# Optimization experiments

Hardware: AMD Instinct MI355X
Metric: run time of the kernel (lower is better)

The kernel has to match this reference:

```python
import jax, jax.numpy as jnp
import numpy as np

D_MODEL = 768
N_HEADS = 12
D_KEYS = 64
D_LLM = 4096
D_INNER = N_HEADS * D_KEYS  # 768


def setup_inputs() -> dict:
    key = jax.random.key(0)
    ks = jax.random.split(key, 12)
    inp = {
        "target_embedding": jax.random.normal(ks[0], (8, 1024, D_MODEL), dtype=jnp.float32),
        "source_embedding": jax.random.normal(ks[1], (1000, D_LLM), dtype=jnp.float32),
        "value_embedding": jax.random.normal(ks[2], (1000, D_LLM), dtype=jnp.float32),
        # Linear params stored as [in, out] (y = x @ W + b)
        "Wq": jax.random.normal(ks[3], (D_MODEL, D_INNER), dtype=jnp.float32) * 0.02,
        "bq": jnp.zeros((D_INNER,), dtype=jnp.float32),
        "Wk": jax.random.normal(ks[4], (D_LLM, D_INNER), dtype=jnp.float32) * 0.02,
        "bk": jnp.zeros((D_INNER,), dtype=jnp.float32),
        "Wv": jax.random.normal(ks[5], (D_LLM, D_INNER), dtype=jnp.float32) * 0.02,
        "bv": jnp.zeros((D_INNER,), dtype=jnp.float32),
        "Wo": jax.random.normal(ks[6], (D_INNER, D_LLM), dtype=jnp.float32) * 0.02,
        "bo": jnp.zeros((D_LLM,), dtype=jnp.float32),
    }
    return inp


def reference(target_embedding, source_embedding, value_embedding,
              Wq, bq, Wk, bk, Wv, bv, Wo, bo):
    B, L, _ = target_embedding.shape
    S, _ = source_embedding.shape
    H, E = N_HEADS, D_KEYS
    # projections
    q = (target_embedding @ Wq + bq).reshape(B, L, H, E)  # [B,L,H,E]
    k = (source_embedding @ Wk + bk).reshape(S, H, E)     # [S,H,E] broadcast over batch
    v = (value_embedding @ Wv + bv).reshape(S, H, E)      # [S,H,E]
    scale = 1.0 / np.sqrt(E).astype(np.float32)
    scores = jnp.einsum('blhe,she->bhls', q, k) * scale   # [B,H,L,S]
    A = jax.nn.softmax(scores, axis=-1)                   # dropout is identity at eval
    out = jnp.einsum('bhls,she->blhe', A, v).reshape(B, L, H * E)
    return out @ Wo + bo                                  # [B,L,d_llm]
```

## Files before the change

### kernel.cpp

```cpp
#include <hip/hip_runtime.h>
#include <cstdint>
#include <type_traits>


typedef unsigned short u16;
typedef __attribute__((ext_vector_type(8))) short bf16x8;
typedef __attribute__((ext_vector_type(4))) float f32x4;
typedef __attribute__((ext_vector_type(16))) float f32x16;
typedef __attribute__((ext_vector_type(4))) float fvec4;
typedef __attribute__((ext_vector_type(4))) unsigned short u16x4;
typedef __attribute__((ext_vector_type(4))) unsigned int u32x4;
typedef __attribute__((ext_vector_type(2))) unsigned int u32x2;

using gld_src_t = const __attribute__((address_space(1))) void*;
using gld_dst_t = __attribute__((address_space(3))) void*;

static __device__ __forceinline__ u16 bf16_rne(float f) {
  uint32_t u = __builtin_bit_cast(uint32_t, f);
  u += 0x7fffu + ((u >> 16) & 1u);
  return (u16)(u >> 16);
}

static __device__ __forceinline__ float exp2_fast(float x) {
  float r; asm("v_exp_f32 %0, %1" : "=v"(r) : "v"(x)); return r;
}

static __device__ __forceinline__ uint32_t pk_bf16(float a, float b) {
  return (uint32_t)bf16_rne(a) | ((uint32_t)bf16_rne(b) << 16);
}

__global__ void convert_pad_bf16(const float* __restrict__ in, u16* __restrict__ out,
                                 int validR, int C, long n4) {
  long stride = (long)gridDim.x * blockDim.x;
  for (long i = (long)blockIdx.x * blockDim.x + threadIdx.x; i < n4; i += stride) {
    long e = i << 2;
    int r = (int)(e / C);
    u16x4 o;
    if (r < validR) {
      fvec4 v = *(const fvec4*)(in + e);
      o[0] = bf16_rne(v[0]); o[1] = bf16_rne(v[1]);
      o[2] = bf16_rne(v[2]); o[3] = bf16_rne(v[3]);
    } else {
      o[0] = 0; o[1] = 0; o[2] = 0; o[3] = 0;
    }
    *(u16x4*)(out + e) = o;
  }
}

template <bool F32IN>
__global__ void transpose_to_bf16(const void* __restrict__ inv, u16* __restrict__ out,
                                  int R, int C) {
  __shared__ u16 tile[32][33];
  int bc = blockIdx.x * 32, br = blockIdx.y * 32;
  int tx = threadIdx.x & 31, ty = threadIdx.x >> 5;
#pragma unroll
  for (int i = 0; i < 4; ++i) {
    int r = br + ty + i * 8, c = bc + tx;
    u16 bits = 0;
    if (r < R && c < C) {
      if constexpr (F32IN) bits = bf16_rne(((const float*)inv)[(size_t)r * C + c]);
      else                 bits = ((const u16*)inv)[(size_t)r * C + c];
    }
    tile[ty + i * 8][tx] = bits;
  }
  __syncthreads();
#pragma unroll
  for (int i = 0; i < 4; ++i) {
    int orow = bc + ty + i * 8, oc = br + tx;
    if (orow < C && oc < R) out[(size_t)orow * R + oc] = tile[tx][ty + i * 8];
  }
}

template <typename CT>
__global__ __launch_bounds__(256) void gemm_bt_128(
    const u16* __restrict__ A0, const u16* __restrict__ A1,
    const u16* __restrict__ B0, const u16* __restrict__ B1,
    const float* __restrict__ bias0, const float* __restrict__ bias1,
    CT* __restrict__ C0, CT* __restrict__ C1,
    int M, int N, int K, float escale) {
  const u16* A = blockIdx.z ? A1 : A0;
  const u16* B = blockIdx.z ? B1 : B0;
  const float* bias = blockIdx.z ? bias1 : bias0;
  CT* C = blockIdx.z ? C1 : C0;
  (void)M;

  __shared__ u16 As[128 * 32];
  __shared__ u16 Bs[128 * 32];

  const int tid = threadIdx.x;
  const int w = tid >> 6, lane = tid & 63;
  const int lr = lane & 15, lg = lane >> 4;
  const int bm = blockIdx.y * 128, bn = blockIdx.x * 128;
  const int wr = (w >> 1) * 64, wc = (w & 1) * 64;

  f32x4 acc[4][4] = {};

  const int nk = K >> 5;
  for (int kt = 0; kt < nk; ++kt) {
#pragma unroll
    for (int j = 0; j < 2; ++j) {
      int cb = j * 256 + w * 64;
      int c = cb + lane;
      const u16* gA = A + (size_t)(bm + (c >> 2)) * K + (size_t)kt * 32 + (c & 3) * 8;
      __builtin_amdgcn_global_load_lds((gld_src_t)(const void*)gA,
                                       (gld_dst_t)(As + (size_t)cb * 8), 16, 0, 0);
      const u16* gB = B + (size_t)(bn + (c >> 2)) * K + (size_t)kt * 32 + (c & 3) * 8;
      __builtin_amdgcn_global_load_lds((gld_src_t)(const void*)gB,
                                       (gld_dst_t)(Bs + (size_t)cb * 8), 16, 0, 0);
    }
    __syncthreads();

    bf16x8 af[4], bfr[4];
#pragma unroll
    for (int m = 0; m < 4; ++m)
      af[m] = *(const bf16x8*)(As + (wr + m * 16 + lr) * 32 + lg * 8);
#pragma unroll
    for (int n = 0; n < 4; ++n)
      bfr[n] = *(const bf16x8*)(Bs + (wc + n * 16 + lr) * 32 + lg * 8);
#pragma unroll
    for (int m = 0; m < 4; ++m)
#pragma unroll
      for (int n = 0; n < 4; ++n)
        acc[m][n] = __builtin_amdgcn_mfma_f32_16x16x32_bf16(af[m], bfr[n], acc[m][n], 0, 0, 0);
    __syncthreads();
  }

#pragma unroll
  for (int n = 0; n < 4; ++n) {
    int col = bn + wc + n * 16 + lr;
    float bv = bias[col];
#pragma unroll
    for (int m = 0; m < 4; ++m) {
      int row0 = bm + wr + m * 16 + lg * 4;
#pragma unroll
      for (int r = 0; r < 4; ++r) {
        float v = (acc[m][n][r] + bv) * escale;
        if constexpr (std::is_same<CT, u16>::value)
          C[(size_t)(row0 + r) * N + col] = bf16_rne(v);
        else
          C[(size_t)(row0 + r) * N + col] = v;
      }
    }
  }
}

__global__ __launch_bounds__(512, 2) void gemm_bt_256(
    const u16* __restrict__ A, const u16* __restrict__ B,
    const float* __restrict__ bias, float* __restrict__ C,
    int M, int N, int K) {
  __shared__ u16 As[2][256 * 64];
  __shared__ u16 Bs[2][256 * 64];
  (void)M;

  const int tid = threadIdx.x, lane = tid & 63, w = tid >> 6;
  const int lr = lane & 15, lg = lane >> 4;
  const int wr = w >> 2, wcol = w & 3;

  const int nbx = N >> 8;
  const int bid = blockIdx.y * gridDim.x + blockIdx.x;
  const int cpx = (gridDim.x * gridDim.y) >> 3;
  const int swz = (bid & 7) * cpx + (bid >> 3);
  const int bm = (swz / nbx) * 256, bn = (swz % nbx) * 256;

  f32x4 acc[8][4] = {};

  auto STAGE = [&](int t, int buf) {
#pragma unroll
    for (int h = 0; h < 2; ++h)
#pragma unroll
      for (int it = 0; it < 2; ++it) {
        const int s = it * 512 + tid;
        const int r = s >> 3;
        const int cg = (s & 7) ^ (r & 7);
        const int row = h * 128 + r;
        const int ldsb = h * 16384 + (it * 512 + w * 64) * 16;
        __builtin_amdgcn_global_load_lds(
            (gld_src_t)(const void*)(A + (size_t)(bm + row) * K + t * 64 + cg * 8),
            (gld_dst_t)((char*)&As[buf][0] + ldsb), 16, 0, 0);
        __builtin_amdgcn_global_load_lds(
            (gld_src_t)(const void*)(B + (size_t)(bn + row) * K + t * 64 + cg * 8),
            (gld_dst_t)((char*)&Bs[buf][0] + ldsb), 16, 0, 0);
      }
  };

  auto LDF = [&](const u16* base, int R, int CB) {
    return *(const bf16x8*)((const char*)base + (size_t)R * 128 + (CB ^ ((R & 7) << 4)));
  };

  STAGE(0, 0);

  const int nk = K >> 6;
  for (int t = 0; t < nk; ++t) {
    const int cur = t & 1;
    if (t + 1 < nk) {
      STAGE(t + 1, cur ^ 1);
      asm volatile("s_waitcnt vmcnt(8)" ::: "memory");
    } else {
      asm volatile("s_waitcnt vmcnt(0)" ::: "memory");
    }
    __builtin_amdgcn_s_barrier();
    __builtin_amdgcn_sched_barrier(0);

    const u16* as = &As[cur][0];
    const u16* bs = &Bs[cur][0];

    bf16x8 bfrag[4][2];
#pragma unroll
    for (int nf = 0; nf < 4; ++nf)
#pragma unroll
      for (int kk = 0; kk < 2; ++kk)
        bfrag[nf][kk] = LDF(bs, wcol * 64 + nf * 16 + lr, kk * 64 + lg * 16);

#pragma unroll
    for (int q = 0; q < 4; ++q) {
      bf16x8 af[2][2];
#pragma unroll
      for (int m2 = 0; m2 < 2; ++m2)
#pragma unroll
        for (int kk = 0; kk < 2; ++kk)
          af[m2][kk] = LDF(as, wr * 128 + (q * 2 + m2) * 16 + lr, kk * 64 + lg * 16);
      __builtin_amdgcn_s_setprio(1);
#pragma unroll
      for (int m2 = 0; m2 < 2; ++m2)
#pragma unroll
        for (int kk = 0; kk < 2; ++kk)
#pragma unroll
          for (int nf = 0; nf < 4; ++nf)
            acc[q * 2 + m2][nf] = __builtin_amdgcn_mfma_f32_16x16x32_bf16(
                af[m2][kk], bfrag[nf][kk], acc[q * 2 + m2][nf], 0, 0, 0);
      __builtin_amdgcn_s_setprio(0);
    }
    __builtin_amdgcn_sched_barrier(0);
    __builtin_amdgcn_s_barrier();
  }

  float bv[4];
#pragma unroll
  for (int nf = 0; nf < 4; ++nf) bv[nf] = bias[bn + wcol * 64 + nf * 16 + lr];
#pragma unroll
  for (int mf = 0; mf < 8; ++mf) {
    const int row0 = bm + wr * 128 + mf * 16 + lg * 4;
#pragma unroll
    for (int nf = 0; nf < 4; ++nf) {
      const int col = bn + wcol * 64 + nf * 16 + lr;
#pragma unroll
      for (int r = 0; r < 4; ++r)
        C[(size_t)(row0 + r) * N + col] = acc[mf][nf][r] + bv[nf];
    }
  }
}

__global__ __launch_bounds__(256) void gemm_kv_splitk(
    const u16* __restrict__ Sb, const u16* __restrict__ Vbi,
    const u16* __restrict__ WkT, const u16* __restrict__ WvT,
    float* __restrict__ part) {
  const int z = blockIdx.z;
  const u16* A = (z >> 2) ? Vbi : Sb;
  const u16* B = (z >> 2) ? WvT : WkT;
  float* C = part + (size_t)z * (1024 * 768);
  const int kofs = (z & 3) * 1024;

  __shared__ u16 As[128 * 32];
  __shared__ u16 Bs[128 * 32];
  const int tid = threadIdx.x, w = tid >> 6, lane = tid & 63;
  const int lr = lane & 15, lg = lane >> 4;
  const int bm = blockIdx.y * 128, bn = blockIdx.x * 128;
  const int wr = (w >> 1) * 64, wc = (w & 1) * 64;
  f32x4 acc[4][4] = {};

  for (int kt = 0; kt < 32; ++kt) {
#pragma unroll
    for (int j = 0; j < 2; ++j) {
      int cb = j * 256 + w * 64;
      int c = cb + lane;
      const u16* gA = A + (size_t)(bm + (c >> 2)) * 4096 + kofs + kt * 32 + (c & 3) * 8;
      __builtin_amdgcn_global_load_lds((gld_src_t)(const void*)gA,
                                       (gld_dst_t)(As + (size_t)cb * 8), 16, 0, 0);
      const u16* gB = B + (size_t)(bn + (c >> 2)) * 4096 + kofs + kt * 32 + (c & 3) * 8;
      __builtin_amdgcn_global_load_lds((gld_src_t)(const void*)gB,
                                       (gld_dst_t)(Bs + (size_t)cb * 8), 16, 0, 0);
    }
    __syncthreads();
    bf16x8 af[4], bfr[4];
#pragma unroll
    for (int m = 0; m < 4; ++m)
      af[m] = *(const bf16x8*)(As + (wr + m * 16 + lr) * 32 + lg * 8);
#pragma unroll
    for (int n = 0; n < 4; ++n)
      bfr[n] = *(const bf16x8*)(Bs + (wc + n * 16 + lr) * 32 + lg * 8);
#pragma unroll
    for (int m = 0; m < 4; ++m)
#pragma unroll
      for (int n = 0; n < 4; ++n)
        acc[m][n] = __builtin_amdgcn_mfma_f32_16x16x32_bf16(af[m], bfr[n], acc[m][n], 0, 0, 0);
    __syncthreads();
  }
#pragma unroll
  for (int n = 0; n < 4; ++n) {
    int col = bn + wc + n * 16 + lr;
#pragma unroll
    for (int m = 0; m < 4; ++m) {
      int row0 = bm + wr + m * 16 + lg * 4;
#pragma unroll
      for (int r = 0; r < 4; ++r)
        C[(size_t)(row0 + r) * 768 + col] = acc[m][n][r];
    }
  }
}

__global__ __launch_bounds__(256) void kv_reduce(const float* __restrict__ part,
                                                 const float* __restrict__ bk,
                                                 const float* __restrict__ bv,
                                                 u16* __restrict__ Kp, u16* __restrict__ Vp) {
  const int mat = blockIdx.y;
  const long e = ((long)blockIdx.x * 256 + threadIdx.x) * 4;
  const float* p0 = part + (size_t)mat * 4 * 786432 + e;
  fvec4 s = *(const fvec4*)p0;
  s += *(const fvec4*)(p0 + 786432);
  s += *(const fvec4*)(p0 + 2 * 786432);
  s += *(const fvec4*)(p0 + 3 * 786432);
  const float* bias = mat ? bv : bk;
  int col = (int)(e % 768);
  fvec4 bb = *(const fvec4*)(bias + col);
  s += bb;
  u16x4 o;
  o[0] = bf16_rne(s[0]); o[1] = bf16_rne(s[1]); o[2] = bf16_rne(s[2]); o[3] = bf16_rne(s[3]);
  u16* dst = mat ? Vp : Kp;
  *(u16x4*)(dst + e) = o;
}

__global__ __launch_bounds__(256, 3) void attn_flash(
    const u16* __restrict__ Q,
    const u16* __restrict__ Kb,
    const u16* __restrict__ VT,
    u16* __restrict__ O) {
  constexpr int DM = 768, SPAD = 1024;
  __shared__ u16 Ks[2][64 * 64];
  __shared__ u16 VTs[2][64 * 64];

  const int tid = threadIdx.x, w = tid >> 6, lane = tid & 63;
  const int q5 = lane & 31, hi = lane >> 5, l7 = lane & 7;
  const int h = blockIdx.y;
  const int qrow = blockIdx.x * 128 + w * 32 + q5;

  bf16x8 qf[4];
#pragma unroll
  for (int dstep = 0; dstep < 4; ++dstep)
    qf[dstep] = *(const bf16x8*)(Q + (size_t)qrow * DM + h * 64 + dstep * 16 + hi * 8);

  auto STAGE = [&](int ch, int buf) {
#pragma unroll
    for (int it = 0; it < 2; ++it) {
      int slot = it * 256 + w * 64 + lane;
      int row = slot >> 3;
      int cg = (slot & 7) ^ (row & 7);
      __builtin_amdgcn_global_load_lds(
          (gld_src_t)(const void*)(Kb + (size_t)(ch * 64 + row) * DM + h * 64 + cg * 8),
          (gld_dst_t)(&Ks[buf][(size_t)(it * 256 + w * 64) * 8]), 16, 0, 0);
      __builtin_amdgcn_global_load_lds(
          (gld_src_t)(const void*)(VT + (size_t)(h * 64 + row) * SPAD + ch * 64 + cg * 8),
          (gld_dst_t)(&VTs[buf][(size_t)(it * 256 + w * 64) * 8]), 16, 0, 0);
    }
  };

  STAGE(0, 0);

  float m_run = -3.0e38f, l_part = 0.0f;
  f32x16 oa0 = {}, oa1 = {};

  for (int ch = 0; ch < 16; ++ch) {
    const int cur = ch & 1;
    if (ch < 15) {
      STAGE(ch + 1, cur ^ 1);
      asm volatile("s_waitcnt vmcnt(4)" ::: "memory");
    } else {
      asm volatile("s_waitcnt vmcnt(0)" ::: "memory");
    }
    __builtin_amdgcn_s_barrier();
    __builtin_amdgcn_sched_barrier(0);

    const char* kbase = (const char*)&Ks[cur][0];
    const char* vbase = (const char*)&VTs[cur][0];

    f32x16 sc0 = {}, sc1 = {};
#pragma unroll
    for (int dstep = 0; dstep < 4; ++dstep) {
      const int colb = (dstep * 32 + hi * 16);
      bf16x8 kf0 = *(const bf16x8*)(kbase + (size_t)q5 * 128 + (colb ^ (l7 << 4)));
      bf16x8 kf1 = *(const bf16x8*)(kbase + (size_t)(32 + q5) * 128 + (colb ^ (l7 << 4)));
      sc0 = __builtin_amdgcn_mfma_f32_32x32x16_bf16(kf0, qf[dstep], sc0, 0, 0, 0);
      sc1 = __builtin_amdgcn_mfma_f32_32x32x16_bf16(kf1, qf[dstep], sc1, 0, 0, 0);
    }
    if (ch == 15) {
#pragma unroll
      for (int r = 4; r < 16; ++r) sc1[r] = -3.0e38f;
    }

    float mi = sc0[0];
#pragma unroll
    for (int r = 1; r < 16; ++r) mi = fmaxf(mi, sc0[r]);
#pragma unroll
    for (int r = 0; r < 16; ++r) mi = fmaxf(mi, sc1[r]);
    float cm = fmaxf(mi, __shfl_xor(mi, 32, 64));

    if (__any(cm > m_run + 8.0f)) {
      float mn = fmaxf(m_run, cm);
      float fsc = exp2_fast(m_run - mn);
      m_run = mn;
      l_part *= fsc;
#pragma unroll
      for (int r = 0; r < 16; ++r) { oa0[r] *= fsc; oa1[r] *= fsc; }
    }

#pragma unroll
    for (int r = 0; r < 16; ++r) {
      float p0 = exp2_fast(sc0[r] - m_run); l_part += p0; sc0[r] = p0;
      float p1 = exp2_fast(sc1[r] - m_run); l_part += p1; sc1[r] = p1;
    }

#pragma unroll
    for (int st = 0; st < 2; ++st) {
#pragma unroll
      for (int ks = 0; ks < 2; ++ks) {
        float pv0, pv1, pv2, pv3, pv4, pv5, pv6, pv7;
        if (st == 0) {
          if (ks == 0) { pv0=sc0[0];pv1=sc0[1];pv2=sc0[2];pv3=sc0[3];pv4=sc0[4];pv5=sc0[5];pv6=sc0[6];pv7=sc0[7]; }
          else         { pv0=sc0[8];pv1=sc0[9];pv2=sc0[10];pv3=sc0[11];pv4=sc0[12];pv5=sc0[13];pv6=sc0[14];pv7=sc0[15]; }
        } else {
          if (ks == 0) { pv0=sc1[0];pv1=sc1[1];pv2=sc1[2];pv3=sc1[3];pv4=sc1[4];pv5=sc1[5];pv6=sc1[6];pv7=sc1[7]; }
          else         { pv0=sc1[8];pv1=sc1[9];pv2=sc1[10];pv3=sc1[11];pv4=sc1[12];pv5=sc1[13];pv6=sc1[14];pv7=sc1[15]; }
        }
        uint32_t a = pk_bf16(pv0, pv1), b = pk_bf16(pv2, pv3);
        uint32_t c = pk_bf16(pv4, pv5), d = pk_bf16(pv6, pv7);
        uint32_t sa = (uint32_t)__shfl_xor((int)a, 32, 64);
        uint32_t sb = (uint32_t)__shfl_xor((int)b, 32, 64);
        uint32_t sc_ = (uint32_t)__shfl_xor((int)c, 32, 64);
        uint32_t sd = (uint32_t)__shfl_xor((int)d, 32, 64);
        u32x4 jw;
        jw[0] = hi ? sc_ : a;
        jw[1] = hi ? sd  : b;
        jw[2] = hi ? c   : sa;
        jw[3] = hi ? d   : sb;
        bf16x8 pB = __builtin_bit_cast(bf16x8, jw);
        const int colb = (st * 64 + ks * 32 + hi * 16);
#pragma unroll
        for (int dt = 0; dt < 2; ++dt) {
          bf16x8 vtf = *(const bf16x8*)(vbase + (size_t)(dt * 32 + q5) * 128 + (colb ^ (l7 << 4)));
          if (dt == 0) oa0 = __builtin_amdgcn_mfma_f32_32x32x16_bf16(vtf, pB, oa0, 0, 0, 0);
          else         oa1 = __builtin_amdgcn_mfma_f32_32x32x16_bf16(vtf, pB, oa1, 0, 0, 0);
        }
      }
    }
    __builtin_amdgcn_sched_barrier(0);
    __builtin_amdgcn_s_barrier();
  }

  float ool = 1.0f / (l_part + __shfl_xor(l_part, 32, 64));
  u16* obase = O + (size_t)qrow * DM + h * 64;
#pragma unroll
  for (int dt = 0; dt < 2; ++dt) {
#pragma unroll
    for (int g = 0; g < 4; ++g) {
      float v0, v1, v2, v3;
      if (dt == 0) { v0 = oa0[4*g]; v1 = oa0[4*g+1]; v2 = oa0[4*g+2]; v3 = oa0[4*g+3]; }
      else         { v0 = oa1[4*g]; v1 = oa1[4*g+1]; v2 = oa1[4*g+2]; v3 = oa1[4*g+3]; }
      u32x2 st2;
      st2[0] = pk_bf16(v0 * ool, v1 * ool);
      st2[1] = pk_bf16(v2 * ool, v3 * ool);
      *(u32x2*)(obase + dt * 32 + g * 8 + hi * 4) = st2;
    }
  }
}

extern "C" void kernel_launch(void* const* d_in, const int* in_sizes, int n_in,
                              void* d_out, int out_size, void* d_ws, size_t ws_size,
                              hipStream_t stream) {
  (void)in_sizes; (void)n_in; (void)out_size; (void)ws_size;
  const float* target = (const float*)d_in[0];
  const float* source = (const float*)d_in[1];
  const float* value  = (const float*)d_in[2];
  const float* Wq = (const float*)d_in[3];
  const float* bq = (const float*)d_in[4];
  const float* Wk = (const float*)d_in[5];
  const float* bk = (const float*)d_in[6];
  const float* Wv = (const float*)d_in[7];
  const float* bv = (const float*)d_in[8];
  const float* Wo = (const float*)d_in[9];
  const float* bo = (const float*)d_in[10];
  float* out = (float*)d_out;

  char* ws = (char*)d_ws;
  size_t off = 0;
  auto carve = [&](size_t bytes) { void* p = ws + off; off += (bytes + 255) & ~(size_t)255; return p; };
  u16* Xb  = (u16*)carve(8192ull * 768 * 2);
  u16* Sb  = (u16*)carve(1024ull * 4096 * 2);
  u16* Vbi = (u16*)carve(1024ull * 4096 * 2);
  u16* WqT = (u16*)carve(768ull * 768 * 2);
  u16* WkT = (u16*)carve(768ull * 4096 * 2);
  u16* WvT = (u16*)carve(768ull * 4096 * 2);
  u16* WoT = (u16*)carve(4096ull * 768 * 2);
  u16* Qb  = (u16*)carve(8192ull * 768 * 2);
  u16* Kp  = (u16*)carve(1024ull * 768 * 2);
  u16* Vp  = (u16*)carve(1024ull * 768 * 2);
  u16* VTp = (u16*)carve(768ull * 1024 * 2);
  u16* Ob  = (u16*)carve(8192ull * 768 * 2);

  const float SCL = 0.18033688011112042f;

  convert_pad_bf16<<<2048, 256, 0, stream>>>(target, Xb, 8192, 768, (8192ll * 768) / 4);
  convert_pad_bf16<<<2048, 256, 0, stream>>>(source, Sb, 1000, 4096, (1024ll * 4096) / 4);
  convert_pad_bf16<<<2048, 256, 0, stream>>>(value,  Vbi, 1000, 4096, (1024ll * 4096) / 4);
  transpose_to_bf16<true><<<dim3(24, 24),  256, 0, stream>>>(Wq, WqT, 768, 768);
  transpose_to_bf16<true><<<dim3(24, 128), 256, 0, stream>>>(Wk, WkT, 4096, 768);
  transpose_to_bf16<true><<<dim3(24, 128), 256, 0, stream>>>(Wv, WvT, 4096, 768);
  transpose_to_bf16<true><<<dim3(128, 24), 256, 0, stream>>>(Wo, WoT, 768, 4096);

  gemm_kv_splitk<<<dim3(6, 8, 8), 256, 0, stream>>>(Sb, Vbi, WkT, WvT, out);
  kv_reduce<<<dim3(768, 2), 256, 0, stream>>>(out, bk, bv, Kp, Vp);
  transpose_to_bf16<false><<<dim3(24, 32), 256, 0, stream>>>(Vp, VTp, 1024, 768);

  gemm_bt_128<u16><<<dim3(6, 64, 1), 256, 0, stream>>>(Xb, Xb, WqT, WqT, bq, bq, Qb, Qb,
                                                       8192, 768, 768, SCL);

  attn_flash<<<dim3(64, 12), 256, 0, stream>>>(Qb, Kp, VTp, Ob);

  gemm_bt_256<<<dim3(16, 32), 512, 0, stream>>>(Ob, WoT, bo, out, 8192, 4096, 768);
}
```

Before: 227.4 us.

## Unify Q and output projections into one pipelined 128x128 double-buffered GEMM

Replaces the unbuffered 128x128 Q-projection GEMM and the 256x256 output-projection GEMM with a single templated 128x128-tile kernel. The new kernel uses a 64-deep K step, double-buffered swizzled LDS, and grid swizzling. The Q projection gains load/compute overlap. The output projection moves to smaller tiles with more blocks, giving better occupancy at the cost of lower data reuse per tile.

Result: no change. 226.6 us (-0.4%).

```diff
diff --git a/kernel.cpp b/kernel.cpp
--- a/kernel.cpp
+++ b/kernel.cpp
@@ -72,115 +72,39 @@
 }
 
 template <typename CT>
-__global__ __launch_bounds__(256) void gemm_bt_128(
-    const u16* __restrict__ A0, const u16* __restrict__ A1,
-    const u16* __restrict__ B0, const u16* __restrict__ B1,
-    const float* __restrict__ bias0, const float* __restrict__ bias1,
-    CT* __restrict__ C0, CT* __restrict__ C1,
-    int M, int N, int K, float escale) {
-  const u16* A = blockIdx.z ? A1 : A0;
-  const u16* B = blockIdx.z ? B1 : B0;
-  const float* bias = blockIdx.z ? bias1 : bias0;
-  CT* C = blockIdx.z ? C1 : C0;
-  (void)M;
-
-  __shared__ u16 As[128 * 32];
-  __shared__ u16 Bs[128 * 32];
-
-  const int tid = threadIdx.x;
-  const int w = tid >> 6, lane = tid & 63;
-  const int lr = lane & 15, lg = lane >> 4;
-  const int bm = blockIdx.y * 128, bn = blockIdx.x * 128;
-  const int wr = (w >> 1) * 64, wc = (w & 1) * 64;
-
-  f32x4 acc[4][4] = {};
-
-  const int nk = K >> 5;
-  for (int kt = 0; kt < nk; ++kt) {
-#pragma unroll
-    for (int j = 0; j < 2; ++j) {
-      int cb = j * 256 + w * 64;
-      int c = cb + lane;
-      const u16* gA = A + (size_t)(bm + (c >> 2)) * K + (size_t)kt * 32 + (c & 3) * 8;
-      __builtin_amdgcn_global_load_lds((gld_src_t)(const void*)gA,
-                                       (gld_dst_t)(As + (size_t)cb * 8), 16, 0, 0);
-      const u16* gB = B + (size_t)(bn + (c >> 2)) * K + (size_t)kt * 32 + (c & 3) * 8;
-      __builtin_amdgcn_global_load_lds((gld_src_t)(const void*)gB,
-                                       (gld_dst_t)(Bs + (size_t)cb * 8), 16, 0, 0);
-    }
-    __syncthreads();
-
-    bf16x8 af[4], bfr[4];
-#pragma unroll
-    for (int m = 0; m < 4; ++m)
-      af[m] = *(const bf16x8*)(As + (wr + m * 16 + lr) * 32 + lg * 8);
-#pragma unroll
-    for (int n = 0; n < 4; ++n)
-      bfr[n] = *(const bf16x8*)(Bs + (wc + n * 16 + lr) * 32 + lg * 8);
-#pragma unroll
-    for (int m = 0; m < 4; ++m)
-#pragma unroll
-      for (int n = 0; n < 4; ++n)
-        acc[m][n] = __builtin_amdgcn_mfma_f32_16x16x32_bf16(af[m], bfr[n], acc[m][n], 0, 0, 0);
-    __syncthreads();
-  }
-
-#pragma unroll
-  for (int n = 0; n < 4; ++n) {
-    int col = bn + wc + n * 16 + lr;
-    float bv = bias[col];
-#pragma unroll
-    for (int m = 0; m < 4; ++m) {
-      int row0 = bm + wr + m * 16 + lg * 4;
-#pragma unroll
-      for (int r = 0; r < 4; ++r) {
-        float v = (acc[m][n][r] + bv) * escale;
-        if constexpr (std::is_same<CT, u16>::value)
-          C[(size_t)(row0 + r) * N + col] = bf16_rne(v);
-        else
-          C[(size_t)(row0 + r) * N + col] = v;
-      }
-    }
-  }
-}
-
-__global__ __launch_bounds__(512, 2) void gemm_bt_256(
+__global__ __launch_bounds__(256, 2) void gemm_bt_128p(
     const u16* __restrict__ A, const u16* __restrict__ B,
-    const float* __restrict__ bias, float* __restrict__ C,
-    int M, int N, int K) {
-  __shared__ u16 As[2][256 * 64];
-  __shared__ u16 Bs[2][256 * 64];
-  (void)M;
+    const float* __restrict__ bias, CT* __restrict__ C,
+    int N, int K, float escale) {
+  __shared__ u16 As[2][128 * 64];
+  __shared__ u16 Bs[2][128 * 64];
 
   const int tid = threadIdx.x, lane = tid & 63, w = tid >> 6;
   const int lr = lane & 15, lg = lane >> 4;
-  const int wr = w >> 2, wcol = w & 3;
-
-  const int nbx = N >> 8;
+  const int wr = (w >> 1) * 64, wc = (w & 1) * 64;
+
+  const int nbx = N >> 7;
   const int bid = blockIdx.y * gridDim.x + blockIdx.x;
   const int cpx = (gridDim.x * gridDim.y) >> 3;
   const int swz = (bid & 7) * cpx + (bid >> 3);
-  const int bm = (swz / nbx) * 256, bn = (swz % nbx) * 256;
-
-  f32x4 acc[8][4] = {};
+  const int bm = (swz / nbx) * 128, bn = (swz % nbx) * 128;
+
+  f32x4 acc[4][4] = {};
 
   auto STAGE = [&](int t, int buf) {
 #pragma unroll
-    for (int h = 0; h < 2; ++h)
-#pragma unroll
-      for (int it = 0; it < 2; ++it) {
-        const int s = it * 512 + tid;
-        const int r = s >> 3;
-        const int cg = (s & 7) ^ (r & 7);
-        const int row = h * 128 + r;
-        const int ldsb = h * 16384 + (it * 512 + w * 64) * 16;
-        __builtin_amdgcn_global_load_lds(
-            (gld_src_t)(const void*)(A + (size_t)(bm + row) * K + t * 64 + cg * 8),
-            (gld_dst_t)((char*)&As[buf][0] + ldsb), 16, 0, 0);
-        __builtin_amdgcn_global_load_lds(
-            (gld_src_t)(const void*)(B + (size_t)(bn + row) * K + t * 64 + cg * 8),
-            (gld_dst_t)((char*)&Bs[buf][0] + ldsb), 16, 0, 0);
-      }
+    for (int it = 0; it < 4; ++it) {
+      const int s = it * 256 + tid;
+      const int r = s >> 3;
+      const int cg = (s & 7) ^ (r & 7);
+      const int ldsb = (it * 256 + w * 64) * 16;
+      __builtin_amdgcn_global_load_lds(
+          (gld_src_t)(const void*)(A + (size_t)(bm + r) * K + t * 64 + cg * 8),
+          (gld_dst_t)((char*)&As[buf][0] + ldsb), 16, 0, 0);
+      __builtin_amdgcn_global_load_lds(
+          (gld_src_t)(const void*)(B + (size_t)(bn + r) * K + t * 64 + cg * 8),
+          (gld_dst_t)((char*)&Bs[buf][0] + ldsb), 16, 0, 0);
+    }
   };
 
   auto LDF = [&](const u16* base, int R, int CB) {
@@ -204,48 +128,48 @@
     const u16* as = &As[cur][0];
     const u16* bs = &Bs[cur][0];
 
-    bf16x8 bfrag[4][2];
-#pragma unroll
-    for (int nf = 0; nf < 4; ++nf)
+    bf16x8 af[4][2], bfr[4][2];
+#pragma unroll
+    for (int m = 0; m < 4; ++m)
 #pragma unroll
       for (int kk = 0; kk < 2; ++kk)
-        bfrag[nf][kk] = LDF(bs, wcol * 64 + nf * 16 + lr, kk * 64 + lg * 16);
-
-#pragma unroll
-    for (int q = 0; q < 4; ++q) {
-      bf16x8 af[2][2];
-#pragma unroll
-      for (int m2 = 0; m2 < 2; ++m2)
-#pragma unroll
-        for (int kk = 0; kk < 2; ++kk)
-          af[m2][kk] = LDF(as, wr * 128 + (q * 2 + m2) * 16 + lr, kk * 64 + lg * 16);
-      __builtin_amdgcn_s_setprio(1);
-#pragma unroll
-      for (int m2 = 0; m2 < 2; ++m2)
-#pragma unroll
-        for (int kk = 0; kk < 2; ++kk)
-#pragma unroll
-          for (int nf = 0; nf < 4; ++nf)
-            acc[q * 2 + m2][nf] = __builtin_amdgcn_mfma_f32_16x16x32_bf16(
-                af[m2][kk], bfrag[nf][kk], acc[q * 2 + m2][nf], 0, 0, 0);
-      __builtin_amdgcn_s_setprio(0);
-    }
+        af[m][kk] = LDF(as, wr + m * 16 + lr, kk * 64 + lg * 16);
+#pragma unroll
+    for (int n = 0; n < 4; ++n)
+#pragma unroll
+      for (int kk = 0; kk < 2; ++kk)
+        bfr[n][kk] = LDF(bs, wc + n * 16 + lr, kk * 64 + lg * 16);
+
+    __builtin_amdgcn_s_setprio(1);
+#pragma unroll
+    for (int kk = 0; kk < 2; ++kk)
+#pragma unroll
+      for (int m = 0; m < 4; ++m)
+#pragma unroll
+        for (int n = 0; n < 4; ++n)
+          acc[m][n] = __builtin_amdgcn_mfma_f32_16x16x32_bf16(
+              af[m][kk], bfr[n][kk], acc[m][n], 0, 0, 0);
+    __builtin_amdgcn_s_setprio(0);
+
     __builtin_amdgcn_sched_barrier(0);
     __builtin_amdgcn_s_barrier();
   }
 
-  float bv[4];
-#pragma unroll
-  for (int nf = 0; nf < 4; ++nf) bv[nf] = bias[bn + wcol * 64 + nf * 16 + lr];
-#pragma unroll
-  for (int mf = 0; mf < 8; ++mf) {
-    const int row0 = bm + wr * 128 + mf * 16 + lg * 4;
-#pragma unroll
-    for (int nf = 0; nf < 4; ++nf) {
-      const int col = bn + wcol * 64 + nf * 16 + lr;
-#pragma unroll
-      for (int r = 0; r < 4; ++r)
-        C[(size_t)(row0 + r) * N + col] = acc[mf][nf][r] + bv[nf];
+#pragma unroll
+  for (int n = 0; n < 4; ++n) {
+    const int col = bn + wc + n * 16 + lr;
+    const float bv = bias[col];
+#pragma unroll
+    for (int m = 0; m < 4; ++m) {
+      const int row0 = bm + wr + m * 16 + lg * 4;
+#pragma unroll
+      for (int r = 0; r < 4; ++r) {
+        float v = (acc[m][n][r] + bv) * escale;
+        if constexpr (std::is_same<CT, u16>::value)
+          C[(size_t)(row0 + r) * N + col] = bf16_rne(v);
+        else
+          C[(size_t)(row0 + r) * N + col] = v;
+      }
     }
   }
 }
@@ -519,10 +443,9 @@
   kv_reduce<<<dim3(768, 2), 256, 0, stream>>>(out, bk, bv, Kp, Vp);
   transpose_to_bf16<false><<<dim3(24, 32), 256, 0, stream>>>(Vp, VTp, 1024, 768);
 
-  gemm_bt_128<u16><<<dim3(6, 64, 1), 256, 0, stream>>>(Xb, Xb, WqT, WqT, bq, bq, Qb, Qb,
-                                                       8192, 768, 768, SCL);
+  gemm_bt_128p<u16><<<dim3(6, 64), 256, 0, stream>>>(Xb, WqT, bq, Qb, 768, 768, SCL);
 
   attn_flash<<<dim3(64, 12), 256, 0, stream>>>(Qb, Kp, VTp, Ob);
 
-  gemm_bt_256<<<dim3(16, 32), 512, 0, stream>>>(Ob, WoT, bo, out, 8192, 4096, 768);
-}
+  gemm_bt_128p<float><<<dim3(32, 64), 256, 0, stream>>>(Ob, WoT, bo, out, 4096, 768, 1.0f);
+}
```
